# Optimization experiments

Measured on AMD Instinct MI355X. Metric: run time of the kernel, lower is better.

Reference implementation:

```python
import jax, jax.numpy as jnp
import numpy as np

ROWS = 256
COLS = 256
EPS = 1e-8


def _radius_bins(rows, cols):
    # Same construction as SpectralLoss.__init__: integer radius per rfft bin,
    # ifftshifted along the row axis to match torch.rfft layout.
    shift_rows = rows // 2
    cols_onesided = cols // 2 + 1
    idx = np.indices((rows, cols_onesided)) - np.array([[[shift_rows]], [[0]]])
    r = np.sqrt(idx[0] ** 2 + idx[1] ** 2).astype(int)
    r = np.fft.ifftshift(r, axes=0)
    return r  # [rows, cols_onesided], values in [0, r_max]


def setup_inputs() -> dict:
    key = jax.random.key(0)
    k1, k2 = jax.random.split(key)
    r = _radius_bins(ROWS, COLS)
    vector_length = int(r.max()) + 1  # 182
    data = jax.random.normal(k1, (128, 3, ROWS, COLS), dtype=jnp.float32)
    mean = jax.random.uniform(k2, (vector_length,), dtype=jnp.float32)
    radius = jnp.asarray(r, dtype=jnp.int32)
    return {"data": data, "mean": mean, "radius": radius}


def reference(data, mean, radius):
    L = mean.shape[0]  # vector_length = r_max + 1
    # RGB -> luma (as in SpectralLoss.fft)
    gray = 0.299 * data[:, 0] + 0.587 * data[:, 1] + 0.114 * data[:, 2]  # [B,H,W]
    f = jnp.fft.rfft2(gray)  # [B, H, W//2+1]
    power = f.real ** 2 + f.imag ** 2  # sum of squared re/im parts
    fft_abs = 20.0 * jnp.log(power + EPS)  # [B, H, Wc]
    # Radial histogram: segment-mean keyed on integer radius (replaces the
    # original dense one-hot mask broadcast of shape [B, L, H, Wc]).
    seg = radius.reshape(-1)  # [N] with N = H*Wc
    B = fft_abs.shape[0]
    flat = fft_abs.reshape(B, -1).T  # [N, B]
    sums = jax.ops.segment_sum(flat, seg, num_segments=L)  # [L, B]
    counts = jax.ops.segment_sum(jnp.ones_like(flat[:, :1]), seg, num_segments=L)  # [L, 1]
    profile = (sums / counts).T  # [B, L]
    # Per-sample min-max normalization (same order of ops as torch code)
    profile = profile - jnp.min(profile, axis=1, keepdims=True)
    profile = profile / jnp.max(profile, axis=1, keepdims=True)
    # L1 loss with reduction='sum' against the target mean profile
    return jnp.sum(jnp.abs(profile - mean[None, :]))
```

## Files before the change

### kernel.cpp

```cpp
#include <hip/hip_runtime.h>
#include <cmath>

#define B_   128
#define H_   256
#define W_   256
#define WC_  129
#define L_   182
#define NG_  33
#define PI_F 3.14159265358979f

__device__ __forceinline__ void fft256_wave(float vr[4], float vi[4], int l) {
  float c0, s0;
  __sincosf(-2.f * PI_F * (float)l / 256.f, &s0, &c0);
  {
    float ur = vr[0] + vr[2], ui = vi[0] + vi[2];
    float dr = vr[0] - vr[2], di = vi[0] - vi[2];
    vr[0] = ur; vi[0] = ui;
    vr[2] = dr * c0 - di * s0; vi[2] = dr * s0 + di * c0;
    float c1 = s0, s1 = -c0;
    ur = vr[1] + vr[3]; ui = vi[1] + vi[3];
    dr = vr[1] - vr[3]; di = vi[1] - vi[3];
    vr[1] = ur; vi[1] = ui;
    vr[3] = dr * c1 - di * s1; vi[3] = dr * s1 + di * c1;
  }
  {
    float c2 = c0 * c0 - s0 * s0, s2 = 2.f * c0 * s0;
    float ur = vr[0] + vr[1], ui = vi[0] + vi[1];
    float dr = vr[0] - vr[1], di = vi[0] - vi[1];
    vr[0] = ur; vi[0] = ui;
    vr[1] = dr * c2 - di * s2; vi[1] = dr * s2 + di * c2;
    ur = vr[2] + vr[3]; ui = vi[2] + vi[3];
    dr = vr[2] - vr[3]; di = vi[2] - vi[3];
    vr[2] = ur; vi[2] = ui;
    vr[3] = dr * c2 - di * s2; vi[3] = dr * s2 + di * c2;
  }
  #pragma unroll
  for (int h = 32; h >= 1; h >>= 1) {
    int i = l & (h - 1);
    float c, s;
    __sincosf(-PI_F * (float)i / (float)h, &s, &c);
    bool up = (l & h) != 0;
    float cc = up ? c : 1.f;
    float ss = up ? s : 0.f;
    float sgn = up ? -1.f : 1.f;
    #pragma unroll
    for (int j = 0; j < 4; ++j) {
      float br = __shfl_xor(vr[j], h, 64);
      float bi = __shfl_xor(vi[j], h, 64);
      float tr = fmaf(sgn, vr[j], br);
      float ti = fmaf(sgn, vi[j], bi);
      vr[j] = tr * cc - ti * ss;
      vi[j] = tr * ss + ti * cc;
    }
  }
}

#define P1_PAIRS 16
#define P1_STRIDE 259

__global__ __launch_bounds__(1024) void pass1_kernel(
    const float* __restrict__ data, float4* __restrict__ inter4) {
  __shared__ float2 tile[P1_PAIRS * P1_STRIDE];
  int tid = threadIdx.x;
  int w = tid >> 6, l = tid & 63;
  int b = blockIdx.x >> 3;
  int row0 = (blockIdx.x & 7) * 32;
  int rowA = row0 + 2 * w;
  const float* pA = data + ((size_t)b * 3) * (H_ * W_) + (size_t)rowA * W_;
  float vr[4], vi[4];
  #pragma unroll
  for (int j = 0; j < 4; ++j) {
    int i = l + 64 * j;
    float r = pA[i], g = pA[H_ * W_ + i], bl = pA[2 * H_ * W_ + i];
    vr[j] = fmaf(0.299f, r, fmaf(0.587f, g, 0.114f * bl));
    r = pA[W_ + i]; g = pA[H_ * W_ + W_ + i]; bl = pA[2 * H_ * W_ + W_ + i];
    vi[j] = fmaf(0.299f, r, fmaf(0.587f, g, 0.114f * bl));
  }
  fft256_wave(vr, vi, l);
  #pragma unroll
  for (int j = 0; j < 4; ++j)
    tile[w * P1_STRIDE + l + 64 * j] = make_float2(vr[j], vi[j]);
  __syncthreads();
  for (int f = tid; f < WC_ * P1_PAIRS; f += 1024) {
    int k = f >> 4;
    int p = f & 15;
    int qk  = (int)(__brev((unsigned)k) >> 24);
    int qnk = (int)(__brev((unsigned)((256 - k) & 255)) >> 24);
    float2 Zk  = tile[p * P1_STRIDE + qk];
    float2 Znk = tile[p * P1_STRIDE + qnk];
    float4 o;
    o.x = 0.5f * (Zk.x + Znk.x);
    o.y = 0.5f * (Zk.y - Znk.y);
    o.z = 0.5f * (Zk.y + Znk.y);
    o.w = 0.5f * (Znk.x - Zk.x);
    inter4[((((size_t)b * WC_ + k) * H_ + row0) >> 1) + p] = o;
  }
}

__global__ __launch_bounds__(256) void pass2_kernel(
    const float2* __restrict__ inter, const int* __restrict__ radius,
    float* __restrict__ partial, float* __restrict__ cntpart) {
  __shared__ float lbins[L_];
  __shared__ float lcnt[L_];
  int tid = threadIdx.x;
  int wv = tid >> 6, l = tid & 63;
  int b = blockIdx.x / NG_;
  int g = blockIdx.x - b * NG_;
  int k = g * 4 + wv;
  bool do_cnt = (b == 0);
  for (int i = tid; i < L_; i += 256) lbins[i] = 0.f;
  if (do_cnt)
    for (int i = tid; i < L_; i += 256) lcnt[i] = 0.f;
  __syncthreads();
  if (k < WC_) {
    const float2* p = inter + ((size_t)b * WC_ + k) * H_;
    float vr[4], vi[4];
    #pragma unroll
    for (int j = 0; j < 4; ++j) {
      float2 v = p[l + 64 * j];
      vr[j] = v.x; vi[j] = v.y;
    }
    fft256_wave(vr, vi, l);
    int rb = 4 * (int)(__brev((unsigned)l) >> 26);
    #pragma unroll
    for (int j = 0; j < 4; ++j) {
      int rf = rb + ((j == 1) ? 2 : (j == 2) ? 1 : j);
      int bin = radius[rf * WC_ + k];
      float pw = vr[j] * vr[j] + vi[j] * vi[j];
      float val = 20.f * __logf(pw + 1e-8f);
      atomicAdd(&lbins[bin], val);
      if (do_cnt) atomicAdd(&lcnt[bin], 1.f);
    }
  }
  __syncthreads();
  float* pp = partial + ((size_t)b * NG_ + g) * L_;
  for (int i = tid; i < L_; i += 256) pp[i] = lbins[i];
  if (do_cnt) {
    float* cp = cntpart + (size_t)g * L_;
    for (int i = tid; i < L_; i += 256) cp[i] = lcnt[i];
  }
}

__global__ __launch_bounds__(256) void loss_kernel(
    const float* __restrict__ partial, const float* __restrict__ cntpart,
    const float* __restrict__ mean, float* __restrict__ lpart) {
  int b = blockIdx.x;
  int t = threadIdx.x;
  __shared__ float prof[L_];
  __shared__ float red[256];
  float acc = 0.f, csum = 0.f;
  if (t < L_) {
    const float* pb = partial + (size_t)b * NG_ * L_;
    #pragma unroll 3
    for (int g = 0; g < NG_; ++g) {
      acc  += pb[g * L_ + t];
      csum += cntpart[g * L_ + t];
    }
    prof[t] = acc / csum;
  }
  __syncthreads();
  red[t] = (t < L_) ? prof[t] : INFINITY;
  __syncthreads();
  for (int s = 128; s > 0; s >>= 1) {
    if (t < s) red[t] = fminf(red[t], red[t + s]);
    __syncthreads();
  }
  float mn = red[0];
  __syncthreads();
  red[t] = (t < L_) ? (prof[t] - mn) : -INFINITY;
  __syncthreads();
  for (int s = 128; s > 0; s >>= 1) {
    if (t < s) red[t] = fmaxf(red[t], red[t + s]);
    __syncthreads();
  }
  float mx = red[0];
  __syncthreads();
  red[t] = (t < L_) ? fabsf((prof[t] - mn) / mx - mean[t]) : 0.f;
  __syncthreads();
  for (int s = 128; s > 0; s >>= 1) {
    if (t < s) red[t] += red[t + s];
    __syncthreads();
  }
  if (t == 0) lpart[b] = red[0];
}

__global__ __launch_bounds__(64) void final_kernel(
    const float* __restrict__ lpart, float* __restrict__ out) {
  int l = threadIdx.x;
  float v = lpart[l] + lpart[l + 64];
  #pragma unroll
  for (int h = 32; h >= 1; h >>= 1) v += __shfl_xor(v, h, 64);
  if (l == 0) out[0] = v;
}

extern "C" void kernel_launch(void* const* d_in, const int* in_sizes, int n_in,
                              void* d_out, int out_size, void* d_ws, size_t ws_size,
                              hipStream_t stream) {
  const float* data   = (const float*)d_in[0];
  const float* mean   = (const float*)d_in[1];
  const int*   radius = (const int*)d_in[2];
  float* out = (float*)d_out;

  float2* inter = (float2*)d_ws;
  size_t inter_bytes = (size_t)B_ * WC_ * H_ * sizeof(float2);
  float* partial = (float*)((char*)d_ws + inter_bytes);
  float* cntpart = partial + (size_t)B_ * NG_ * L_;
  float* lpart   = cntpart + (size_t)NG_ * L_;

  pass1_kernel<<<B_ * 8, 1024, 0, stream>>>(data, (float4*)inter);
  pass2_kernel<<<B_ * NG_, 256, 0, stream>>>(inter, radius, partial, cntpart);
  loss_kernel<<<B_, 256, 0, stream>>>(partial, cntpart, mean, lpart);
  final_kernel<<<1, 64, 0, stream>>>(lpart, out);
}
```

Measured before the change: 194.3 us.

## Fuse row and column FFT passes into one kernel with an LDS-resident spectrum

Replaces the two-pass pipeline with a single kernel per half-image. It computes row FFTs, keeps the needed half-spectrum columns in shared memory, then runs column FFTs and the radial binning without the global intermediate buffer. This removes the large write and read of the intermediate spectrum and one kernel launch, and shrinks the partial-sum reduction to two groups. In exchange it drops the two-real-rows-per-complex-FFT trick. Both blocks of an image also redo the full row FFTs and read the input twice, so there is more arithmetic and only 256 large blocks with heavy LDS use.

```diff
diff --git a/kernel.cpp b/kernel.cpp
--- a/kernel.cpp
+++ b/kernel.cpp
@@ -6,33 +6,33 @@
 #define W_   256
 #define WC_  129
 #define L_   182
-#define NG_  33
+#define NS0  65
+#define SPEC_PAD 257
 #define PI_F 3.14159265358979f
 
-__device__ __forceinline__ void fft256_wave(float vr[4], float vi[4], int l) {
+__device__ __forceinline__ void fft256x2_wave(float vr[8], float vi[8], int l) {
   float c0, s0;
   __sincosf(-2.f * PI_F * (float)l / 256.f, &s0, &c0);
-  {
-    float ur = vr[0] + vr[2], ui = vi[0] + vi[2];
-    float dr = vr[0] - vr[2], di = vi[0] - vi[2];
-    vr[0] = ur; vi[0] = ui;
-    vr[2] = dr * c0 - di * s0; vi[2] = dr * s0 + di * c0;
-    float c1 = s0, s1 = -c0;
-    ur = vr[1] + vr[3]; ui = vi[1] + vi[3];
-    dr = vr[1] - vr[3]; di = vi[1] - vi[3];
-    vr[1] = ur; vi[1] = ui;
-    vr[3] = dr * c1 - di * s1; vi[3] = dr * s1 + di * c1;
-  }
-  {
-    float c2 = c0 * c0 - s0 * s0, s2 = 2.f * c0 * s0;
-    float ur = vr[0] + vr[1], ui = vi[0] + vi[1];
-    float dr = vr[0] - vr[1], di = vi[0] - vi[1];
-    vr[0] = ur; vi[0] = ui;
-    vr[1] = dr * c2 - di * s2; vi[1] = dr * s2 + di * c2;
-    ur = vr[2] + vr[3]; ui = vi[2] + vi[3];
-    dr = vr[2] - vr[3]; di = vi[2] - vi[3];
-    vr[2] = ur; vi[2] = ui;
-    vr[3] = dr * c2 - di * s2; vi[3] = dr * s2 + di * c2;
+  float c1 = s0, s1 = -c0;
+  float c2 = c0 * c0 - s0 * s0, s2 = 2.f * c0 * s0;
+  #pragma unroll
+  for (int f = 0; f < 8; f += 4) {
+    float ur = vr[f+0] + vr[f+2], ui = vi[f+0] + vi[f+2];
+    float dr = vr[f+0] - vr[f+2], di = vi[f+0] - vi[f+2];
+    vr[f+0] = ur; vi[f+0] = ui;
+    vr[f+2] = dr * c0 - di * s0; vi[f+2] = dr * s0 + di * c0;
+    ur = vr[f+1] + vr[f+3]; ui = vi[f+1] + vi[f+3];
+    dr = vr[f+1] - vr[f+3]; di = vi[f+1] - vi[f+3];
+    vr[f+1] = ur; vi[f+1] = ui;
+    vr[f+3] = dr * c1 - di * s1; vi[f+3] = dr * s1 + di * c1;
+    ur = vr[f+0] + vr[f+1]; ui = vi[f+0] + vi[f+1];
+    dr = vr[f+0] - vr[f+1]; di = vi[f+0] - vi[f+1];
+    vr[f+0] = ur; vi[f+0] = ui;
+    vr[f+1] = dr * c2 - di * s2; vi[f+1] = dr * s2 + di * c2;
+    ur = vr[f+2] + vr[f+3]; ui = vi[f+2] + vi[f+3];
+    dr = vr[f+2] - vr[f+3]; di = vi[f+2] - vi[f+3];
+    vr[f+2] = ur; vi[f+2] = ui;
+    vr[f+3] = dr * c2 - di * s2; vi[f+3] = dr * s2 + di * c2;
   }
   #pragma unroll
   for (int h = 32; h >= 1; h >>= 1) {
@@ -44,7 +44,7 @@
     float ss = up ? s : 0.f;
     float sgn = up ? -1.f : 1.f;
     #pragma unroll
-    for (int j = 0; j < 4; ++j) {
+    for (int j = 0; j < 8; ++j) {
       float br = __shfl_xor(vr[j], h, 64);
       float bi = __shfl_xor(vi[j], h, 64);
       float tr = fmaf(sgn, vr[j], br);
@@ -55,89 +55,97 @@
   }
 }
 
-#define P1_PAIRS 16
-#define P1_STRIDE 259
-
-__global__ __launch_bounds__(1024) void pass1_kernel(
-    const float* __restrict__ data, float4* __restrict__ inter4) {
-  __shared__ float2 tile[P1_PAIRS * P1_STRIDE];
-  int tid = threadIdx.x;
-  int w = tid >> 6, l = tid & 63;
-  int b = blockIdx.x >> 3;
-  int row0 = (blockIdx.x & 7) * 32;
-  int rowA = row0 + 2 * w;
-  const float* pA = data + ((size_t)b * 3) * (H_ * W_) + (size_t)rowA * W_;
-  float vr[4], vi[4];
-  #pragma unroll
-  for (int j = 0; j < 4; ++j) {
-    int i = l + 64 * j;
-    float r = pA[i], g = pA[H_ * W_ + i], bl = pA[2 * H_ * W_ + i];
-    vr[j] = fmaf(0.299f, r, fmaf(0.587f, g, 0.114f * bl));
-    r = pA[W_ + i]; g = pA[H_ * W_ + W_ + i]; bl = pA[2 * H_ * W_ + W_ + i];
-    vi[j] = fmaf(0.299f, r, fmaf(0.587f, g, 0.114f * bl));
-  }
-  fft256_wave(vr, vi, l);
-  #pragma unroll
-  for (int j = 0; j < 4; ++j)
-    tile[w * P1_STRIDE + l + 64 * j] = make_float2(vr[j], vi[j]);
-  __syncthreads();
-  for (int f = tid; f < WC_ * P1_PAIRS; f += 1024) {
-    int k = f >> 4;
-    int p = f & 15;
-    int qk  = (int)(__brev((unsigned)k) >> 24);
-    int qnk = (int)(__brev((unsigned)((256 - k) & 255)) >> 24);
-    float2 Zk  = tile[p * P1_STRIDE + qk];
-    float2 Znk = tile[p * P1_STRIDE + qnk];
-    float4 o;
-    o.x = 0.5f * (Zk.x + Znk.x);
-    o.y = 0.5f * (Zk.y - Znk.y);
-    o.z = 0.5f * (Zk.y + Znk.y);
-    o.w = 0.5f * (Znk.x - Zk.x);
-    inter4[((((size_t)b * WC_ + k) * H_ + row0) >> 1) + p] = o;
-  }
-}
-
-__global__ __launch_bounds__(256) void pass2_kernel(
-    const float2* __restrict__ inter, const int* __restrict__ radius,
+__global__ __launch_bounds__(1024) void mega_kernel(
+    const float* __restrict__ data, const int* __restrict__ radius,
     float* __restrict__ partial, float* __restrict__ cntpart) {
+  __shared__ float specR[NS0 * SPEC_PAD];
+  __shared__ float specI[NS0 * SPEC_PAD];
   __shared__ float lbins[L_];
   __shared__ float lcnt[L_];
   int tid = threadIdx.x;
-  int wv = tid >> 6, l = tid & 63;
-  int b = blockIdx.x / NG_;
-  int g = blockIdx.x - b * NG_;
-  int k = g * 4 + wv;
+  int w = tid >> 6, l = tid & 63;
+  int b = blockIdx.x >> 1;
+  int c = blockIdx.x & 1;
+  int s_base = c ? NS0 : 0;
+  int ns = c ? (WC_ - NS0) : NS0;
   bool do_cnt = (b == 0);
-  for (int i = tid; i < L_; i += 256) lbins[i] = 0.f;
-  if (do_cnt)
-    for (int i = tid; i < L_; i += 256) lcnt[i] = 0.f;
-  __syncthreads();
-  if (k < WC_) {
-    const float2* p = inter + ((size_t)b * WC_ + k) * H_;
-    float vr[4], vi[4];
-    #pragma unroll
-    for (int j = 0; j < 4; ++j) {
-      float2 v = p[l + 64 * j];
-      vr[j] = v.x; vi[j] = v.y;
-    }
-    fft256_wave(vr, vi, l);
+  for (int i = tid; i < L_; i += 1024) { lbins[i] = 0.f; lcnt[i] = 0.f; }
+  const float* base = data + (size_t)b * 3 * (H_ * W_);
+
+  for (int t = 0; t < 8; ++t) {
+    int yA = t * 32 + w;
+    int yB = yA + 16;
+    const float* pA = base + (size_t)yA * W_;
+    const float* pB = base + (size_t)yB * W_;
+    float vr[8], vi[8];
+    #pragma unroll
+    for (int j = 0; j < 4; ++j) {
+      int x = l + 64 * j;
+      float r = pA[x], g = pA[H_ * W_ + x], bl = pA[2 * H_ * W_ + x];
+      vr[j] = fmaf(0.299f, r, fmaf(0.587f, g, 0.114f * bl));
+      vi[j] = 0.f;
+      r = pB[x]; g = pB[H_ * W_ + x]; bl = pB[2 * H_ * W_ + x];
+      vr[4 + j] = fmaf(0.299f, r, fmaf(0.587f, g, 0.114f * bl));
+      vi[4 + j] = 0.f;
+    }
+    fft256x2_wave(vr, vi, l);
+    #pragma unroll
+    for (int j = 0; j < 4; ++j) {
+      int q = l + 64 * j;
+      int s = (q & 1) ? ((q == 1) ? 128 : -1) : (q >> 1);
+      if (s >= s_base && s < s_base + ns) {
+        int sl = s - s_base;
+        specR[sl * SPEC_PAD + yA] = vr[j];
+        specI[sl * SPEC_PAD + yA] = vi[j];
+        specR[sl * SPEC_PAD + yB] = vr[4 + j];
+        specI[sl * SPEC_PAD + yB] = vi[4 + j];
+      }
+    }
+  }
+  __syncthreads();
+
+  for (int t = 0; t < 3; ++t) {
+    int sA = t * 32 + w;
+    int sB = sA + 16;
+    bool vA = sA < ns, vB = sB < ns;
+    int eA = vA ? sA : 0, eB = vB ? sB : 0;
+    float vr[8], vi[8];
+    #pragma unroll
+    for (int j = 0; j < 4; ++j) {
+      int y = l + 64 * j;
+      vr[j]     = specR[eA * SPEC_PAD + y];
+      vi[j]     = specI[eA * SPEC_PAD + y];
+      vr[4 + j] = specR[eB * SPEC_PAD + y];
+      vi[4 + j] = specI[eB * SPEC_PAD + y];
+    }
+    fft256x2_wave(vr, vi, l);
+    int sgA = s_base + eA, sgB = s_base + eB;
+    int kxA = (sgA == 128) ? 128 : (int)(__brev((unsigned)(2 * sgA)) >> 24);
+    int kxB = (sgB == 128) ? 128 : (int)(__brev((unsigned)(2 * sgB)) >> 24);
     int rb = 4 * (int)(__brev((unsigned)l) >> 26);
     #pragma unroll
     for (int j = 0; j < 4; ++j) {
-      int rf = rb + ((j == 1) ? 2 : (j == 2) ? 1 : j);
-      int bin = radius[rf * WC_ + k];
-      float pw = vr[j] * vr[j] + vi[j] * vi[j];
-      float val = 20.f * __logf(pw + 1e-8f);
-      atomicAdd(&lbins[bin], val);
-      if (do_cnt) atomicAdd(&lcnt[bin], 1.f);
-    }
-  }
-  __syncthreads();
-  float* pp = partial + ((size_t)b * NG_ + g) * L_;
-  for (int i = tid; i < L_; i += 256) pp[i] = lbins[i];
+      int ky = rb + ((j == 1) ? 2 : (j == 2) ? 1 : j);
+      if (vA) {
+        int bin = radius[ky * WC_ + kxA];
+        float pw = vr[j] * vr[j] + vi[j] * vi[j];
+        atomicAdd(&lbins[bin], 20.f * __logf(pw + 1e-8f));
+        if (do_cnt) atomicAdd(&lcnt[bin], 1.f);
+      }
+      if (vB) {
+        int bin = radius[ky * WC_ + kxB];
+        float pw = vr[4 + j] * vr[4 + j] + vi[4 + j] * vi[4 + j];
+        atomicAdd(&lbins[bin], 20.f * __logf(pw + 1e-8f));
+        if (do_cnt) atomicAdd(&lcnt[bin], 1.f);
+      }
+    }
+  }
+  __syncthreads();
+  float* pp = partial + ((size_t)b * 2 + c) * L_;
+  for (int i = tid; i < L_; i += 1024) pp[i] = lbins[i];
   if (do_cnt) {
-    float* cp = cntpart + (size_t)g * L_;
-    for (int i = tid; i < L_; i += 256) cp[i] = lcnt[i];
+    float* cp = cntpart + (size_t)c * L_;
+    for (int i = tid; i < L_; i += 1024) cp[i] = lcnt[i];
   }
 }
 
@@ -148,14 +156,10 @@
   int t = threadIdx.x;
   __shared__ float prof[L_];
   __shared__ float red[256];
-  float acc = 0.f, csum = 0.f;
   if (t < L_) {
-    const float* pb = partial + (size_t)b * NG_ * L_;
-    #pragma unroll 3
-    for (int g = 0; g < NG_; ++g) {
-      acc  += pb[g * L_ + t];
-      csum += cntpart[g * L_ + t];
-    }
+    const float* pb = partial + (size_t)b * 2 * L_;
+    float acc  = pb[t] + pb[L_ + t];
+    float csum = cntpart[t] + cntpart[L_ + t];
     prof[t] = acc / csum;
   }
   __syncthreads();
@@ -201,14 +205,11 @@
   const int*   radius = (const int*)d_in[2];
   float* out = (float*)d_out;
 
-  float2* inter = (float2*)d_ws;
-  size_t inter_bytes = (size_t)B_ * WC_ * H_ * sizeof(float2);
-  float* partial = (float*)((char*)d_ws + inter_bytes);
-  float* cntpart = partial + (size_t)B_ * NG_ * L_;
-  float* lpart   = cntpart + (size_t)NG_ * L_;
-
-  pass1_kernel<<<B_ * 8, 1024, 0, stream>>>(data, (float4*)inter);
-  pass2_kernel<<<B_ * NG_, 256, 0, stream>>>(inter, radius, partial, cntpart);
+  float* partial = (float*)d_ws;
+  float* cntpart = partial + (size_t)B_ * 2 * L_;
+  float* lpart   = cntpart + (size_t)2 * L_;
+
+  mega_kernel<<<B_ * 2, 1024, 0, stream>>>(data, radius, partial, cntpart);
   loss_kernel<<<B_, 256, 0, stream>>>(partial, cntpart, mean, lpart);
   final_kernel<<<1, 64, 0, stream>>>(lpart, out);
 }
```

Measured after the change: 214.1 us. 10.2% more time.
